# Performance work log

Hardware: AMD Instinct MI355X
Metric: run time of the kernel (lower is better)

Reference implementation:

```python
import jax, jax.numpy as jnp
import numpy as np

EPS = 1e-8


def setup_inputs() -> dict:
    key = jax.random.key(0)
    ks = jax.random.split(key, 9)
    b, f, n1, n2 = 32, 256, 64, 256
    inp = {
        "search_feats": jax.random.normal(ks[0], (b, f, n2), jnp.float32),
        "template_feats": jax.random.normal(ks[1], (b, f, n1), jnp.float32),
        "template_seeds": jax.random.normal(ks[2], (b, n1, 3), jnp.float32),
        # SharedMLP (1x1 conv2d) weights: channels 260 -> 256 -> 256 -> 256
        "W1": jax.random.normal(ks[3], (256, 260), jnp.float32) * 0.05,
        "b1": jnp.zeros((256,), jnp.float32),
        "W2": jax.random.normal(ks[4], (256, 256), jnp.float32) * 0.05,
        "b2": jnp.zeros((256,), jnp.float32),
        "W3": jax.random.normal(ks[5], (256, 256), jnp.float32) * 0.05,
        "b3": jnp.zeros((256,), jnp.float32),
        # conv1d chain (kernel size 1): 256 -> 256 (ReLU) -> 256 (no act)
        "W4": jax.random.normal(ks[6], (256, 256), jnp.float32) * 0.05,
        "b4": jnp.zeros((256,), jnp.float32),
        "W5": jax.random.normal(ks[7], (256, 256), jnp.float32) * 0.05,
        "b5": jnp.zeros((256,), jnp.float32),
    }
    return inp


def reference(search_feats, template_feats, template_seeds,
              W1, b1, W2, b2, W3, b3, W4, b4, W5, b5):
    b, f, n2 = search_feats.shape
    n1 = template_feats.shape[-1]

    # Cosine similarity along feature dim (torch clamps each norm to eps).
    t_norm = template_feats / jnp.maximum(
        jnp.linalg.norm(template_feats, axis=1, keepdims=True), EPS)
    s_norm = search_feats / jnp.maximum(
        jnp.linalg.norm(search_feats, axis=1, keepdims=True), EPS)
    sim = jnp.einsum('bfn,bfm->bnm', t_norm, s_norm)  # (b, n1, n2)

    # Build fusion feature (b, 1+3+f, n1, n2) via broadcasting (no copies needed).
    xyz = jnp.transpose(template_seeds, (0, 2, 1))  # (b, 3, n1)
    xyz_b = jnp.broadcast_to(xyz[:, :, :, None], (b, 3, n1, n2))
    tf_b = jnp.broadcast_to(template_feats[:, :, :, None], (b, f, n1, n2))
    fusion = jnp.concatenate([sim[:, None], xyz_b, tf_b], axis=1)  # (b, 260, n1, n2)

    # SharedMLP: 1x1 conv2d + ReLU per layer
    x = jax.nn.relu(jnp.einsum('oc,bcnm->bonm', W1, fusion) + b1[None, :, None, None])
    x = jax.nn.relu(jnp.einsum('oc,bcnm->bonm', W2, x) + b2[None, :, None, None])
    x = jax.nn.relu(jnp.einsum('oc,bcnm->bonm', W3, x) + b3[None, :, None, None])

    # max_pool2d over n1 dim (kernel [n1, 1]) then squeeze -> (b, 256, n2)
    x = jnp.max(x, axis=2)

    # conv1d chain (kernel size 1)
    x = jax.nn.relu(jnp.einsum('oc,bcm->bom', W4, x) + b4[None, :, None])
    x = jnp.einsum('oc,bcm->bom', W5, x) + b5[None, :, None]
    return x
```

## Files before the change

kernel.cpp:

```cpp
#include <hip/hip_runtime.h>
#include <math.h>

#define BB 32
#define FF 256
#define N1 64
#define N2 256

typedef _Float16 f16;
typedef _Float16 f16x4 __attribute__((ext_vector_type(4)));
typedef _Float16 f16x8 __attribute__((ext_vector_type(8)));
typedef float f32x4 __attribute__((ext_vector_type(4)));

#define OFFB_W14T 0u
#define OFFB_W1H  45056u
#define OFFB_W2H  176128u
#define OFFB_W3H  307200u
#define OFFB_W4H  438272u
#define OFFB_W5H  569344u

__global__ void k_prep(const float* __restrict__ W1, const float* __restrict__ W2,
                       const float* __restrict__ W3, const float* __restrict__ W4,
                       const float* __restrict__ W5, char* __restrict__ wsb) {
  int x = blockIdx.x, m = blockIdx.y, t = threadIdx.x;
  int idx = x * 256 + t;
  if (m == 0)      ((f16*)(wsb + OFFB_W2H))[idx] = (f16)W2[idx];
  else if (m == 1) ((f16*)(wsb + OFFB_W3H))[idx] = (f16)W3[idx];
  else if (m == 2) ((f16*)(wsb + OFFB_W4H))[idx] = (f16)W4[idx];
  else if (m == 3) ((f16*)(wsb + OFFB_W5H))[idx] = (f16)W5[idx];
  else if (m == 4) ((f16*)(wsb + OFFB_W1H))[idx] = (f16)W1[x * 260 + 4 + t];
  else if (x < 4)  ((float*)(wsb + OFFB_W14T))[x * 256 + t] = W1[t * 260 + x];
}


#define ZERO_ACC                                                  \
  _Pragma("unroll") for (int of = 0; of < 2; ++of)                \
  _Pragma("unroll") for (int mf = 0; mf < 2; ++mf)                \
      acc[of][mf] = (f32x4){0.f, 0.f, 0.f, 0.f};

#define GEMM2(SRC)                                                                \
  {                                                                               \
    f16x8 bfa0 = *(const f16x8*)((SRC) + 0 * 1024 + lane * 16);                   \
    f16x8 bfa1 = *(const f16x8*)((SRC) + 1 * 1024 + lane * 16);                   \
    _Pragma("unroll") for (int ks = 0; ks < 8; ++ks) {                            \
      f16x8 bfb0 = bfa0, bfb1 = bfa1;                                             \
      if (ks < 7) {                                                               \
        bfb0 = *(const f16x8*)((SRC) + ((ks + 1) * 2 + 0) * 1024 + lane * 16);    \
        bfb1 = *(const f16x8*)((SRC) + ((ks + 1) * 2 + 1) * 1024 + lane * 16);    \
      }                                                                           \
      _Pragma("unroll") for (int of = 0; of < 2; ++of) {                          \
        acc[of][0] = __builtin_amdgcn_mfma_f32_16x16x32_f16(wreg[of][ks], bfa0,   \
                                                            acc[of][0], 0, 0, 0); \
        acc[of][1] = __builtin_amdgcn_mfma_f32_16x16x32_f16(wreg[of][ks], bfa1,   \
                                                            acc[of][1], 0, 0, 0); \
      }                                                                           \
      bfa0 = bfb0; bfa1 = bfb1;                                                   \
    }                                                                             \
  }

#define STORE_FRAG(DST)                                                           \
  _Pragma("unroll") for (int of = 0; of < 2; ++of)                                \
  _Pragma("unroll") for (int mf = 0; mf < 2; ++mf) {                              \
    f16x4 hv;                                                                     \
    _Pragma("unroll") for (int j = 0; j < 4; ++j)                                 \
        hv[j] = (f16)fmaxf(acc[of][mf][j] + biasv[of][j], 0.f);                   \
    *(f16x4*)((DST) + (wg * 2 + mf) * 1024 + (of * 2 + (g >> 1)) * 256 +          \
              r * 16 + (g & 1) * 8) = hv;                                         \
  }

#define POOLUP                                                                    \
  _Pragma("unroll") for (int of = 0; of < 2; ++of)                                \
  _Pragma("unroll") for (int mf = 0; mf < 2; ++mf)                                \
  _Pragma("unroll") for (int j = 0; j < 4; ++j) {                                 \
    f16 hv = (f16)fmaxf(acc[of][mf][j] + biasv[of][j], 0.f);                      \
    if (hv > pool[of][mf][j]) pool[of][mf][j] = hv;                               \
  }

#define PRODUCE_Y1(NN, DST)                                                       \
  {                                                                               \
    float simv = sml[(NN) * 32 + mp * 16 + r];                                    \
    f16x8 c8 = *(const f16x8*)(c1h + (NN) * 264 + kp * 32 + g * 8);               \
    f16x8 h;                                                                      \
    _Pragma("unroll") for (int q = 0; q < 4; ++q) {                               \
      h[q] = (f16)fmaxf(fmaf(w1a[q], simv, (float)c8[q]), 0.f);                   \
      h[4 + q] = (f16)fmaxf(fmaf(w1b[q], simv, (float)c8[4 + q]), 0.f);           \
    }                                                                             \
    *(f16x8*)((DST) + w * 1024 + lane * 16) = h;                                  \
  }

__global__ __launch_bounds__(1024, 4) void k_mega(
    const float* __restrict__ sf, const float* __restrict__ tf,
    const float* __restrict__ seeds, const float* __restrict__ b1,
    const float* __restrict__ b2, const float* __restrict__ b3,
    const float* __restrict__ b4, const float* __restrict__ b5,
    const char* __restrict__ wsb, float* __restrict__ out) {
  const int mt = blockIdx.x, b = blockIdx.y, mb = mt * 32;
  const int tid = threadIdx.x;
  const int w = tid >> 6, lane = tid & 63, g = lane >> 4, r = lane & 15;
  const int grp = w >> 3, wg = w & 7;
  const int kp = w >> 1, mp = w & 1;

  const float* w14t = (const float*)(wsb + OFFB_W14T);
  const f16* w1h = (const f16*)(wsb + OFFB_W1H);
  const f16* w2h = (const f16*)(wsb + OFFB_W2H);
  const f16* w3h = (const f16*)(wsb + OFFB_W3H);
  const f16* w4h = (const f16*)(wsb + OFFB_W4H);
  const f16* w5h = (const f16*)(wsb + OFFB_W5H);

  __shared__ __align__(16) char arena[107904];
#define Y1BUF(i) (arena + (i) * 16384)
#define Y2BUF(i) (arena + 32768 + (i) * 16384)
  f16* c1h = (f16*)(arena + 65536);
  float* sml = (float*)(arena + 99328);
  float* invt_l = (float*)(arena + 107520);
  float* invs_l = (float*)(arena + 107776);
  float* part_t = (float*)(arena + 49152);
  float* part_s = (float*)(arena + 53248);

  {
    const int n = tid & 63, fo = tid >> 6;
    float ssq = 0.f;
#pragma unroll
    for (int j = 0; j < 2; ++j) {
      int oct = j * 16 + fo;
      f16x8 h;
#pragma unroll
      for (int e = 0; e < 8; ++e) {
        float v = tf[((size_t)b * FF + oct * 8 + e) * N1 + n];
        ssq = fmaf(v, v, ssq);
        h[e] = (f16)v;
      }
      *(f16x8*)(arena + ((oct >> 2) * 4 + (n >> 4)) * 1024 +
                ((oct & 3) * 16 + (n & 15)) * 16) = h;
    }
    part_t[n * 16 + fo] = ssq;
  }
  {
    const int m = tid & 31, q = tid >> 5;
    float ssq = 0.f;
    f16x8 h;
#pragma unroll
    for (int e = 0; e < 8; ++e) {
      float v = sf[((size_t)b * FF + q * 8 + e) * N2 + mb + m];
      ssq = fmaf(v, v, ssq);
      h[e] = (f16)v;
    }
    *(f16x8*)(arena + 32768 + ((q >> 2) * 2 + (m >> 4)) * 1024 +
              ((q & 3) * 16 + (m & 15)) * 16) = h;
    part_s[m * 32 + q] = ssq;
  }
  __syncthreads();
  if (tid < 64) {
    float a = 0.f;
#pragma unroll
    for (int i = 0; i < 16; ++i) a += part_t[tid * 16 + i];
    invt_l[tid] = 1.0f / fmaxf(sqrtf(a), 1e-8f);
  }
  if (tid < 32) {
    float a = 0.f;
#pragma unroll
    for (int i = 0; i < 32; ++i) a += part_s[tid * 32 + i];
    invs_l[tid] = 1.0f / fmaxf(sqrtf(a), 1e-8f);
  }
  __syncthreads();

  if (w < 8) {
    const int nt = w >> 1, mfs = w & 1;
    f32x4 sa = {0.f, 0.f, 0.f, 0.f};
#pragma unroll
    for (int ks = 0; ks < 8; ++ks) {
      f16x8 af = *(const f16x8*)(arena + (ks * 4 + nt) * 1024 + lane * 16);
      f16x8 bfm = *(const f16x8*)(arena + 32768 + (ks * 2 + mfs) * 1024 + lane * 16);
      sa = __builtin_amdgcn_mfma_f32_16x16x32_f16(af, bfm, sa, 0, 0, 0);
    }
    float ivm = invs_l[mfs * 16 + r];
#pragma unroll
    for (int j = 0; j < 4; ++j) {
      int n = nt * 16 + g * 4 + j;
      sml[n * 32 + mfs * 16 + r] = sa[j] * invt_l[n] * ivm;
    }
  }
  {
    f16x8 w1f[8];
#pragma unroll
    for (int ks = 0; ks < 8; ++ks)
      w1f[ks] = *(const f16x8*)(w1h + (w * 16 + r) * 256 + ks * 32 + g * 8);
    f32x4 ac[4];
#pragma unroll
    for (int nf = 0; nf < 4; ++nf) ac[nf] = (f32x4){0.f, 0.f, 0.f, 0.f};
#pragma unroll
    for (int ks = 0; ks < 8; ++ks)
#pragma unroll
      for (int nf = 0; nf < 4; ++nf) {
        f16x8 bfm = *(const f16x8*)(arena + (ks * 4 + nf) * 1024 + lane * 16);
        ac[nf] = __builtin_amdgcn_mfma_f32_16x16x32_f16(w1f[ks], bfm, ac[nf], 0, 0, 0);
      }
    f32x4 b1v = *(const f32x4*)(b1 + w * 16 + g * 4);
    f32x4 wx = *(const f32x4*)(w14t + 256 + w * 16 + g * 4);
    f32x4 wy = *(const f32x4*)(w14t + 512 + w * 16 + g * 4);
    f32x4 wz = *(const f32x4*)(w14t + 768 + w * 16 + g * 4);
#pragma unroll
    for (int nf = 0; nf < 4; ++nf) {
      int n = nf * 16 + r;
      const float* sd = seeds + ((size_t)b * 64 + n) * 3;
      float sx = sd[0], sy = sd[1], sz = sd[2];
      f16x4 hv;
#pragma unroll
      for (int j = 0; j < 4; ++j)
        hv[j] = (f16)(ac[nf][j] + b1v[j] + wx[j] * sx + wy[j] * sy + wz[j] * sz);
      *(f16x4*)(c1h + n * 264 + w * 16 + g * 4) = hv;
    }
  }
  __syncthreads();

  f16x8 wreg[2][8];
  f32x4 biasv[2];
  f16x4 pool[2][2];
  f32x4 acc[2][2];
  f32x4 w1a, w1b;
  {
    const f16* wsrc = grp ? w3h : w2h;
    const float* bsrc = grp ? b3 : b2;
#pragma unroll
    for (int of = 0; of < 2; ++of) {
#pragma unroll
      for (int ks = 0; ks < 8; ++ks)
        wreg[of][ks] = *(const f16x8*)(wsrc + (wg * 32 + of * 16 + r) * 256 +
                                       ks * 32 + g * 8);
      biasv[of] = *(const f32x4*)(bsrc + wg * 32 + of * 16 + g * 4);
    }
    w1a = *(const f32x4*)(w14t + kp * 32 + g * 8);
    w1b = *(const f32x4*)(w14t + kp * 32 + g * 8 + 4);
  }
#pragma unroll
  for (int of = 0; of < 2; ++of)
#pragma unroll
    for (int mf = 0; mf < 2; ++mf) pool[of][mf] = (f16x4){0, 0, 0, 0};

  PRODUCE_Y1(0, Y1BUF(0));
  __syncthreads();

  for (int n = 0; n < N1; ++n) {
    if (grp == 0) {
      ZERO_ACC;
      GEMM2(Y1BUF(n & 1));
      STORE_FRAG(Y2BUF(n & 1));
      if (n + 1 < N1) PRODUCE_Y1(n + 1, Y1BUF((n + 1) & 1));
    } else {
      if (n + 1 < N1) PRODUCE_Y1(n + 1, Y1BUF((n + 1) & 1));
      if (n > 0) {
        ZERO_ACC;
        GEMM2(Y2BUF((n - 1) & 1));
        POOLUP;
      }
    }
    __syncthreads();
  }

  if (grp == 1) {
    ZERO_ACC;
    GEMM2(Y2BUF(1));
    POOLUP;
#pragma unroll
    for (int of = 0; of < 2; ++of)
#pragma unroll
      for (int mf = 0; mf < 2; ++mf)
        *(f16x4*)(Y1BUF(0) + (wg * 2 + mf) * 1024 + (of * 2 + (g >> 1)) * 256 +
                  r * 16 + (g & 1) * 8) = pool[of][mf];
  } else {
#pragma unroll
    for (int of = 0; of < 2; ++of) {
#pragma unroll
      for (int ks = 0; ks < 8; ++ks)
        wreg[of][ks] = *(const f16x8*)(w4h + (wg * 32 + of * 16 + r) * 256 +
                                       ks * 32 + g * 8);
      biasv[of] = *(const f32x4*)(b4 + wg * 32 + of * 16 + g * 4);
    }
  }
  __syncthreads();
  if (grp == 0) {
    ZERO_ACC;
    GEMM2(Y1BUF(0));
    STORE_FRAG(Y2BUF(0));
  } else {
#pragma unroll
    for (int of = 0; of < 2; ++of) {
#pragma unroll
      for (int ks = 0; ks < 8; ++ks)
        wreg[of][ks] = *(const f16x8*)(w5h + (wg * 32 + of * 16 + r) * 256 +
                                       ks * 32 + g * 8);
      biasv[of] = *(const f32x4*)(b5 + wg * 32 + of * 16 + g * 4);
    }
  }
  __syncthreads();
  if (grp == 1) {
    ZERO_ACC;
    GEMM2(Y2BUF(0));
#pragma unroll
    for (int of = 0; of < 2; ++of)
#pragma unroll
      for (int mf = 0; mf < 2; ++mf) {
        float* op = out + ((size_t)(b * 256 + wg * 32 + of * 16 + g * 4)) * 256 +
                    mb + mf * 16 + r;
#pragma unroll
        for (int j = 0; j < 4; ++j)
          op[(size_t)j * 256] = acc[of][mf][j] + biasv[of][j];
      }
  }
}

extern "C" void kernel_launch(void* const* d_in, const int* in_sizes, int n_in,
                              void* d_out, int out_size, void* d_ws, size_t ws_size,
                              hipStream_t stream) {
  const float* sf = (const float*)d_in[0];
  const float* tf = (const float*)d_in[1];
  const float* seeds = (const float*)d_in[2];
  const float* W1 = (const float*)d_in[3];
  const float* b1 = (const float*)d_in[4];
  const float* W2 = (const float*)d_in[5];
  const float* b2 = (const float*)d_in[6];
  const float* W3 = (const float*)d_in[7];
  const float* b3 = (const float*)d_in[8];
  const float* W4 = (const float*)d_in[9];
  const float* b4 = (const float*)d_in[10];
  const float* W5 = (const float*)d_in[11];
  const float* b5 = (const float*)d_in[12];
  char* wsb = (char*)d_ws;
  float* out = (float*)d_out;

  k_prep<<<dim3(256, 6), 256, 0, stream>>>(W1, W2, W3, W4, W5, wsb);
  k_mega<<<dim3(8, BB), 1024, 0, stream>>>(sf, tf, seeds, b1, b2, b3, b4, b5,
                                           wsb, out);
}
```

Before: 143.8 us.

## Drop weight prep kernel and convert fp32 weights to fp16 inside mega kernel

Removes the separate k_prep launch that converted W1–W5 to fp16 in workspace. The mega kernel now reads the fp32 weights directly and converts them in registers, including strided loads of the first W1 columns and splitting the W1 GEMM into two halves to limit register use. It also raises wave priority around the MFMA loops with s_setprio. This saves one kernel launch and a workspace round trip, at the cost of twice the global weight bytes per block and strided scalar loads for W1 columns.

```diff
diff --git a/kernel.cpp b/kernel.cpp
--- a/kernel.cpp
+++ b/kernel.cpp
@@ -11,26 +11,18 @@
 typedef _Float16 f16x8 __attribute__((ext_vector_type(8)));
 typedef float f32x4 __attribute__((ext_vector_type(4)));
 
-#define OFFB_W14T 0u
-#define OFFB_W1H  45056u
-#define OFFB_W2H  176128u
-#define OFFB_W3H  307200u
-#define OFFB_W4H  438272u
-#define OFFB_W5H  569344u
-
-__global__ void k_prep(const float* __restrict__ W1, const float* __restrict__ W2,
-                       const float* __restrict__ W3, const float* __restrict__ W4,
-                       const float* __restrict__ W5, char* __restrict__ wsb) {
-  int x = blockIdx.x, m = blockIdx.y, t = threadIdx.x;
-  int idx = x * 256 + t;
-  if (m == 0)      ((f16*)(wsb + OFFB_W2H))[idx] = (f16)W2[idx];
-  else if (m == 1) ((f16*)(wsb + OFFB_W3H))[idx] = (f16)W3[idx];
-  else if (m == 2) ((f16*)(wsb + OFFB_W4H))[idx] = (f16)W4[idx];
-  else if (m == 3) ((f16*)(wsb + OFFB_W5H))[idx] = (f16)W5[idx];
-  else if (m == 4) ((f16*)(wsb + OFFB_W1H))[idx] = (f16)W1[x * 260 + 4 + t];
-  else if (x < 4)  ((float*)(wsb + OFFB_W14T))[x * 256 + t] = W1[t * 260 + x];
-}
-
+
+#define LOADWF(DST, SRCPTR)                                                       \
+  {                                                                               \
+    f32x4 lo_ = *(const f32x4*)(SRCPTR);                                          \
+    f32x4 hi_ = *(const f32x4*)((SRCPTR) + 4);                                    \
+    f16x8 h_;                                                                     \
+    _Pragma("unroll") for (int q_ = 0; q_ < 4; ++q_) {                            \
+      h_[q_] = (f16)lo_[q_];                                                      \
+      h_[4 + q_] = (f16)hi_[q_];                                                  \
+    }                                                                             \
+    DST = h_;                                                                     \
+  }
 
 #define ZERO_ACC                                                  \
   _Pragma("unroll") for (int of = 0; of < 2; ++of)                \
@@ -41,6 +33,7 @@
   {                                                                               \
     f16x8 bfa0 = *(const f16x8*)((SRC) + 0 * 1024 + lane * 16);                   \
     f16x8 bfa1 = *(const f16x8*)((SRC) + 1 * 1024 + lane * 16);                   \
+    __builtin_amdgcn_s_setprio(1);                                                \
     _Pragma("unroll") for (int ks = 0; ks < 8; ++ks) {                            \
       f16x8 bfb0 = bfa0, bfb1 = bfa1;                                             \
       if (ks < 7) {                                                               \
@@ -55,6 +48,17 @@
       }                                                                           \
       bfa0 = bfb0; bfa1 = bfb1;                                                   \
     }                                                                             \
+    __builtin_amdgcn_s_setprio(0);                                                \
+  }
+
+#define LOAD_WREG(WSRC, BSRC)                                                     \
+  _Pragma("unroll") for (int of = 0; of < 2; ++of) {                              \
+    _Pragma("unroll") for (int ks = 0; ks < 8; ++ks) {                            \
+      const float* wp_ = (WSRC) + (size_t)(wg * 32 + of * 16 + r) * 256 +         \
+                         ks * 32 + g * 8;                                         \
+      LOADWF(wreg[of][ks], wp_);                                                  \
+    }                                                                             \
+    biasv[of] = *(const f32x4*)((BSRC) + wg * 32 + of * 16 + g * 4);              \
   }
 
 #define STORE_FRAG(DST)                                                           \
@@ -89,22 +93,17 @@
 
 __global__ __launch_bounds__(1024, 4) void k_mega(
     const float* __restrict__ sf, const float* __restrict__ tf,
-    const float* __restrict__ seeds, const float* __restrict__ b1,
-    const float* __restrict__ b2, const float* __restrict__ b3,
-    const float* __restrict__ b4, const float* __restrict__ b5,
-    const char* __restrict__ wsb, float* __restrict__ out) {
+    const float* __restrict__ seeds, const float* __restrict__ W1,
+    const float* __restrict__ b1, const float* __restrict__ W2,
+    const float* __restrict__ b2, const float* __restrict__ W3,
+    const float* __restrict__ b3, const float* __restrict__ W4,
+    const float* __restrict__ b4, const float* __restrict__ W5,
+    const float* __restrict__ b5, float* __restrict__ out) {
   const int mt = blockIdx.x, b = blockIdx.y, mb = mt * 32;
   const int tid = threadIdx.x;
   const int w = tid >> 6, lane = tid & 63, g = lane >> 4, r = lane & 15;
   const int grp = w >> 3, wg = w & 7;
   const int kp = w >> 1, mp = w & 1;
-
-  const float* w14t = (const float*)(wsb + OFFB_W14T);
-  const f16* w1h = (const f16*)(wsb + OFFB_W1H);
-  const f16* w2h = (const f16*)(wsb + OFFB_W2H);
-  const f16* w3h = (const f16*)(wsb + OFFB_W3H);
-  const f16* w4h = (const f16*)(wsb + OFFB_W4H);
-  const f16* w5h = (const f16*)(wsb + OFFB_W5H);
 
   __shared__ __align__(16) char arena[107904];
 #define Y1BUF(i) (arena + (i) * 16384)
@@ -180,24 +179,36 @@
     }
   }
   {
-    f16x8 w1f[8];
-#pragma unroll
-    for (int ks = 0; ks < 8; ++ks)
-      w1f[ks] = *(const f16x8*)(w1h + (w * 16 + r) * 256 + ks * 32 + g * 8);
     f32x4 ac[4];
 #pragma unroll
     for (int nf = 0; nf < 4; ++nf) ac[nf] = (f32x4){0.f, 0.f, 0.f, 0.f};
-#pragma unroll
-    for (int ks = 0; ks < 8; ++ks)
-#pragma unroll
-      for (int nf = 0; nf < 4; ++nf) {
-        f16x8 bfm = *(const f16x8*)(arena + (ks * 4 + nf) * 1024 + lane * 16);
-        ac[nf] = __builtin_amdgcn_mfma_f32_16x16x32_f16(w1f[ks], bfm, ac[nf], 0, 0, 0);
+#pragma unroll 1
+    for (int half = 0; half < 2; ++half) {
+      f16x8 w1f[4];
+#pragma unroll
+      for (int kk = 0; kk < 4; ++kk) {
+        const float* wp = W1 + (size_t)(w * 16 + r) * 260 + 4 +
+                          (half * 4 + kk) * 32 + g * 8;
+        LOADWF(w1f[kk], wp);
       }
-    f32x4 b1v = *(const f32x4*)(b1 + w * 16 + g * 4);
-    f32x4 wx = *(const f32x4*)(w14t + 256 + w * 16 + g * 4);
-    f32x4 wy = *(const f32x4*)(w14t + 512 + w * 16 + g * 4);
-    f32x4 wz = *(const f32x4*)(w14t + 768 + w * 16 + g * 4);
+#pragma unroll
+      for (int kk = 0; kk < 4; ++kk)
+#pragma unroll
+        for (int nf = 0; nf < 4; ++nf) {
+          f16x8 bfm = *(const f16x8*)(arena + ((half * 4 + kk) * 4 + nf) * 1024 +
+                                      lane * 16);
+          ac[nf] =
+              __builtin_amdgcn_mfma_f32_16x16x32_f16(w1f[kk], bfm, ac[nf], 0, 0, 0);
+        }
+    }
+    float b1v[4], wx[4], wy[4], wz[4];
+#pragma unroll
+    for (int j = 0; j < 4; ++j) {
+      int o = w * 16 + g * 4 + j;
+      b1v[j] = b1[o];
+      const float* wp = W1 + (size_t)o * 260;
+      wx[j] = wp[1]; wy[j] = wp[2]; wz[j] = wp[3];
+    }
 #pragma unroll
     for (int nf = 0; nf < 4; ++nf) {
       int n = nf * 16 + r;
@@ -217,19 +228,13 @@
   f16x4 pool[2][2];
   f32x4 acc[2][2];
   f32x4 w1a, w1b;
+  if (grp) { LOAD_WREG(W3, b3); } else { LOAD_WREG(W2, b2); }
   {
-    const f16* wsrc = grp ? w3h : w2h;
-    const float* bsrc = grp ? b3 : b2;
-#pragma unroll
-    for (int of = 0; of < 2; ++of) {
-#pragma unroll
-      for (int ks = 0; ks < 8; ++ks)
-        wreg[of][ks] = *(const f16x8*)(wsrc + (wg * 32 + of * 16 + r) * 256 +
-                                       ks * 32 + g * 8);
-      biasv[of] = *(const f32x4*)(bsrc + wg * 32 + of * 16 + g * 4);
-    }
-    w1a = *(const f32x4*)(w14t + kp * 32 + g * 8);
-    w1b = *(const f32x4*)(w14t + kp * 32 + g * 8 + 4);
+#pragma unroll
+    for (int q = 0; q < 4; ++q) {
+      w1a[q] = W1[(size_t)(kp * 32 + g * 8 + q) * 260];
+      w1b[q] = W1[(size_t)(kp * 32 + g * 8 + 4 + q) * 260];
+    }
   }
 #pragma unroll
   for (int of = 0; of < 2; ++of)
@@ -267,14 +272,7 @@
         *(f16x4*)(Y1BUF(0) + (wg * 2 + mf) * 1024 + (of * 2 + (g >> 1)) * 256 +
                   r * 16 + (g & 1) * 8) = pool[of][mf];
   } else {
-#pragma unroll
-    for (int of = 0; of < 2; ++of) {
-#pragma unroll
-      for (int ks = 0; ks < 8; ++ks)
-        wreg[of][ks] = *(const f16x8*)(w4h + (wg * 32 + of * 16 + r) * 256 +
-                                       ks * 32 + g * 8);
-      biasv[of] = *(const f32x4*)(b4 + wg * 32 + of * 16 + g * 4);
-    }
+    LOAD_WREG(W4, b4);
   }
   __syncthreads();
   if (grp == 0) {
@@ -282,14 +280,7 @@
     GEMM2(Y1BUF(0));
     STORE_FRAG(Y2BUF(0));
   } else {
-#pragma unroll
-    for (int of = 0; of < 2; ++of) {
-#pragma unroll
-      for (int ks = 0; ks < 8; ++ks)
-        wreg[of][ks] = *(const f16x8*)(w5h + (wg * 32 + of * 16 + r) * 256 +
-                                       ks * 32 + g * 8);
-      biasv[of] = *(const f32x4*)(b5 + wg * 32 + of * 16 + g * 4);
-    }
+    LOAD_WREG(W5, b5);
   }
   __syncthreads();
   if (grp == 1) {
@@ -324,10 +315,8 @@
   const float* b4 = (const float*)d_in[10];
   const float* W5 = (const float*)d_in[11];
   const float* b5 = (const float*)d_in[12];
-  char* wsb = (char*)d_ws;
   float* out = (float*)d_out;
 
-  k_prep<<<dim3(256, 6), 256, 0, stream>>>(W1, W2, W3, W4, W5, wsb);
-  k_mega<<<dim3(8, BB), 1024, 0, stream>>>(sf, tf, seeds, b1, b2, b3, b4, b5,
-                                           wsb, out);
+  k_mega<<<dim3(8, BB), 1024, 0, stream>>>(sf, tf, seeds, W1, b1, W2, b2, W3, b3,
+                                           W4, b4, W5, b5, out);
 }
```

Result: slower. 155.6 us (+8.2%).
